# Kernel optimization log

Hardware: AMD Instinct MI355X
Metric: run time of the kernel (lower is better)

## Reference

```python
import jax, jax.numpy as jnp
import numpy as np

N = 131072   # total nodes in batch
D = 128      # hidden dim (in_dim = out_dim = 128)
DX = 64      # raw node feature dim (x and rw_feature each)
NG = 1024    # number of graphs (global_add_pool segments)
E = 4194304  # edges per hop adjacency (avg degree 32)
H = 4        # num_hops + 1 MLP branches per layer


def setup_inputs() -> dict:
    key = jax.random.key(0)
    ks = jax.random.split(key, 16)
    s = 0.05
    return {
        "x": jax.random.normal(ks[0], (N, DX), jnp.float32),
        "rw_feature": jax.random.normal(ks[1], (N, DX), jnp.float32),
        "hop1_features": jax.random.normal(ks[2], (N, D), jnp.float32),
        "hop2_features": jax.random.normal(ks[3], (N, D), jnp.float32),
        "hop3_features": jax.random.normal(ks[4], (N, D), jnp.float32),
        "hop1_edges": jax.random.randint(ks[5], (2, E), 0, N, dtype=jnp.int32),
        "hop2_edges": jax.random.randint(ks[6], (2, E), 0, N, dtype=jnp.int32),
        "hop3_edges": jax.random.randint(ks[7], (2, E), 0, N, dtype=jnp.int32),
        "batch": jnp.sort(jax.random.randint(ks[8], (N,), 0, NG, dtype=jnp.int32)),
        "l1_w1": jax.random.normal(ks[9], (H, D, D), jnp.float32) * s,
        "l1_b1": jnp.zeros((H, D), jnp.float32),
        "l1_w2": jax.random.normal(ks[10], (H, D, D), jnp.float32) * s,
        "l1_b2": jnp.zeros((H, D), jnp.float32),
        "l2_w1": jax.random.normal(ks[11], (H, D, D), jnp.float32) * s,
        "l2_b1": jnp.zeros((H, D), jnp.float32),
        "l2_w2": jax.random.normal(ks[12], (H, D, D), jnp.float32) * s,
        "l2_b2": jnp.zeros((H, D), jnp.float32),
        "lin_w": jax.random.normal(ks[13], (2 * D, D), jnp.float32) * s,
        "lin_b": jnp.zeros((D,), jnp.float32),
    }


def _mhc_layer(hops, w1, b1, w2, b2):
    # hops: [H, N, D]; per-hop MLP (Linear -> ReLU -> Dropout(eval) -> Linear), summed over hops
    z = jax.nn.relu(jnp.einsum('hni,hio->hno', hops, w1) + b1[:, None, :])
    y = jnp.einsum('hno,hop->hnp', z, w2) + b2[:, None, :]
    return jnp.sum(y, axis=0)  # [N, D]


def _spmm(edges, x):
    # torch.sparse.mm(A, x) with A[r, c] = 1.0 per edge; duplicate edges accumulate (COO sum)
    return jax.ops.segment_sum(x[edges[1]], edges[0], num_segments=N)


def reference(x, rw_feature, hop1_features, hop2_features, hop3_features,
              hop1_edges, hop2_edges, hop3_edges, batch,
              l1_w1, l1_b1, l1_w2, l1_b2, l2_w1, l2_b1, l2_w2, l2_b2,
              lin_w, lin_b):
    f = jnp.concatenate([x, rw_feature], axis=1)  # [N, D]
    h1 = jnp.stack([f, hop1_features, hop2_features, hop3_features], axis=0)  # [H, N, D]
    x1 = _mhc_layer(h1, l1_w1, l1_b1, l1_w2, l1_b2)
    h2 = jnp.stack([x1,
                    _spmm(hop1_edges, x1),
                    _spmm(hop2_edges, x1),
                    _spmm(hop3_edges, x1)], axis=0)
    x2 = _mhc_layer(h2, l2_w1, l2_b1, l2_w2, l2_b2)
    out = jnp.concatenate([x1, x2], axis=1) @ lin_w + lin_b  # concat=True path
    return jax.ops.segment_sum(out, batch, num_segments=NG)  # global_add_pool -> [NG, D]
```

## Files before the change

kernel.cpp:

```cpp
#include <hip/hip_runtime.h>

#define N_NODES 131072
#define DIM     128
#define NGRAPH  1024
#define NEDGE   4194304

#define NW      512
#define WBINS   256
#define NSL     256
#define SLICE_E (NEDGE / NSL)
#define CAP     12288

typedef float floatx4 __attribute__((ext_vector_type(4)));
typedef float f32x4  __attribute__((ext_vector_type(4)));
typedef __bf16 bf16x8 __attribute__((ext_vector_type(8)));
typedef __bf16 bf16x4 __attribute__((ext_vector_type(4)));

__device__ __forceinline__ int lds_off(int row, int kb) {
    return row * 256 + (kb ^ ((row & 7) << 4));
}

__global__ __launch_bounds__(256)
void zero_kernel(floatx4* __restrict__ p, long n4) {
    long i = (long)blockIdx.x * blockDim.x + threadIdx.x;
    long stride = (long)gridDim.x * blockDim.x;
    floatx4 z = {0.f, 0.f, 0.f, 0.f};
    for (; i < n4; i += stride) p[i] = z;
}

__global__ __launch_bounds__(256)
void tr_kernel(const float* __restrict__ src, __bf16* __restrict__ dst, int nmat) {
    int idx = blockIdx.x * blockDim.x + threadIdx.x;
    int total = nmat * 16384;
    if (idx >= total) return;
    int m = idx >> 14;
    int col = (idx >> 7) & 127;
    int k = idx & 127;
    dst[idx] = (__bf16)src[m * 16384 + k * 128 + col];
}

__global__ __launch_bounds__(256)
void wincount_kernel(const int* __restrict__ e1, const int* __restrict__ e2,
                     const int* __restrict__ e3, int* __restrict__ gcount) {
    const int gb = blockIdx.x;
    const int sl = gb % NSL;
    const int hop = gb / NSL;
    const int* rows = hop == 0 ? e1 : hop == 1 ? e2 : e3;

    __shared__ int cnt[NW];
    for (int i = threadIdx.x; i < NW; i += 256) cnt[i] = 0;
    __syncthreads();

    const int4* src = (const int4*)rows + (size_t)sl * (SLICE_E / 4);
    for (int j = threadIdx.x; j < SLICE_E / 4; j += 256) {
        int4 v = src[j];
        atomicAdd(&cnt[v.x >> 8], 1); atomicAdd(&cnt[v.y >> 8], 1);
        atomicAdd(&cnt[v.z >> 8], 1); atomicAdd(&cnt[v.w >> 8], 1);
    }
    __syncthreads();

    int* dst = gcount + ((size_t)hop * NSL + sl) * NW;
    for (int i = threadIdx.x; i < NW; i += 256) dst[i] = cnt[i];
}

__global__ __launch_bounds__(256)
void basescan_kernel(const int* __restrict__ gcount, int* __restrict__ baseo,
                     int* __restrict__ wbase) {
    const int hop = blockIdx.x;
    const int t = threadIdx.x;
    __shared__ int wt[NW];
    __shared__ int part[256];

    for (int k = 0; k < 2; ++k) {
        int w = t * 2 + k;
        int s = 0;
        for (int sl = 0; sl < NSL; ++sl)
            s += gcount[((size_t)hop * NSL + sl) * NW + w];
        wt[w] = s;
    }
    __syncthreads();
    part[t] = wt[2 * t] + wt[2 * t + 1];
    __syncthreads();
    for (int d = 1; d < 256; d <<= 1) {
        int v = (t >= d) ? part[t - d] : 0;
        __syncthreads();
        part[t] += v;
        __syncthreads();
    }
    int run = (t == 0) ? 0 : part[t - 1];
    for (int k = 0; k < 2; ++k) {
        int w = 2 * t + k;
        wbase[hop * (NW + 1) + w] = run;
        int r2 = run;
        for (int sl = 0; sl < NSL; ++sl) {
            baseo[((size_t)hop * NW + w) * NSL + sl] = r2;
            r2 += gcount[((size_t)hop * NSL + sl) * NW + w];
        }
        run += wt[w];
    }
    if (t == 255) wbase[hop * (NW + 1) + NW] = NEDGE;
}

__global__ __launch_bounds__(256)
void bucket_kernel(const int* __restrict__ e1, const int* __restrict__ e2,
                   const int* __restrict__ e3, const int* __restrict__ baseo,
                   int* __restrict__ buf) {
    const int gb = blockIdx.x;
    const int sl = gb % NSL;
    const int hop = gb / NSL;
    const int* rows = hop == 0 ? e1 : hop == 1 ? e2 : e3;
    const int* cs = rows + NEDGE;

    __shared__ int cur[NW];
    for (int i = threadIdx.x; i < NW; i += 256)
        cur[i] = baseo[((size_t)hop * NW + i) * NSL + sl];
    __syncthreads();

    int* b = buf + (size_t)hop * NEDGE;
    const int4* r4 = (const int4*)rows + (size_t)sl * (SLICE_E / 4);
    const int4* c4 = (const int4*)cs + (size_t)sl * (SLICE_E / 4);
    for (int j = threadIdx.x; j < SLICE_E / 4; j += 256) {
        int4 r = r4[j];
        int4 c = c4[j];
        int p;
        p = atomicAdd(&cur[r.x >> 8], 1); b[p] = ((r.x & 255) << 17) | c.x;
        p = atomicAdd(&cur[r.y >> 8], 1); b[p] = ((r.y & 255) << 17) | c.y;
        p = atomicAdd(&cur[r.z >> 8], 1); b[p] = ((r.z & 255) << 17) | c.z;
        p = atomicAdd(&cur[r.w >> 8], 1); b[p] = ((r.w & 255) << 17) | c.w;
    }
}

__global__ __launch_bounds__(256)
void winbuild_kernel(const int* __restrict__ buf, const int* __restrict__ wbase,
                     int* __restrict__ offs3, int* __restrict__ cols) {
    const int gb = blockIdx.x;
    const int w = gb % NW;
    const int hop = gb / NW;
    const int b0 = wbase[hop * (NW + 1) + w];
    const int b1 = wbase[hop * (NW + 1) + w + 1];
    const int tot = b1 - b0;
    const int* src = buf + (size_t)hop * NEDGE + b0;
    int* col = cols + (size_t)hop * NEDGE;
    int* offs = offs3 + (size_t)hop * (N_NODES + 1);
    const int t = threadIdx.x;

    __shared__ int hist[WBINS];
    __shared__ int scanb[WBINS];
    __shared__ int image[CAP];

    hist[t] = 0;
    __syncthreads();
    for (int i = t; i < tot; i += 256) atomicAdd(&hist[src[i] >> 17], 1);
    __syncthreads();

    int v = hist[t];
    scanb[t] = v;
    __syncthreads();
    for (int d = 1; d < 256; d <<= 1) {
        int u = (t >= d) ? scanb[t - d] : 0;
        __syncthreads();
        scanb[t] += u;
        __syncthreads();
    }
    const int excl = scanb[t] - v;

    offs[w * WBINS + t] = b0 + excl;
    if (w == NW - 1 && t == 0) offs[N_NODES] = NEDGE;
    __syncthreads();

    if (tot <= CAP) {
        hist[t] = excl;
        __syncthreads();
        for (int i = t; i < tot; i += 256) {
            int e = src[i];
            int p = atomicAdd(&hist[e >> 17], 1);
            image[p] = e & 0x1FFFF;
        }
        __syncthreads();
        for (int i = t; i < tot; i += 256) col[b0 + i] = image[i];
    } else {
        hist[t] = b0 + excl;
        __syncthreads();
        for (int i = t; i < tot; i += 256) {
            int e = src[i];
            int p = atomicAdd(&hist[e >> 17], 1);
            col[p] = e & 0x1FFFF;
        }
    }
}

__global__ __launch_bounds__(256)
void csr_spmm_kernel(const int* __restrict__ offs, const int* __restrict__ col,
                     const __bf16* __restrict__ xin, __bf16* __restrict__ outb) {
    const int lane = threadIdx.x & 63;
    const int row = blockIdx.x * (blockDim.x >> 6) + (threadIdx.x >> 6);
    if (row >= N_NODES) return;
    const int beg = offs[row];
    const int end = offs[row + 1];

    float a0 = 0.f, a1 = 0.f, b0 = 0.f, b1 = 0.f;
    float c0f = 0.f, c1f = 0.f, d0 = 0.f, d1 = 0.f;
    for (int b = beg; b < end; b += 64) {
        const int n = min(64, end - b);
        int cidx = (b + lane < end) ? col[b + lane] : 0;
        int i = 0;
        for (; i + 4 <= n; i += 4) {
            int e0 = __shfl(cidx, i);
            int e1 = __shfl(cidx, i + 1);
            int e2 = __shfl(cidx, i + 2);
            int e3 = __shfl(cidx, i + 3);
            unsigned v0 = *(const unsigned*)(xin + (size_t)e0 * 128 + lane * 2);
            unsigned v1 = *(const unsigned*)(xin + (size_t)e1 * 128 + lane * 2);
            unsigned v2 = *(const unsigned*)(xin + (size_t)e2 * 128 + lane * 2);
            unsigned v3 = *(const unsigned*)(xin + (size_t)e3 * 128 + lane * 2);
            a0 += __uint_as_float(v0 << 16); a1 += __uint_as_float(v0 & 0xffff0000u);
            b0 += __uint_as_float(v1 << 16); b1 += __uint_as_float(v1 & 0xffff0000u);
            c0f += __uint_as_float(v2 << 16); c1f += __uint_as_float(v2 & 0xffff0000u);
            d0 += __uint_as_float(v3 << 16); d1 += __uint_as_float(v3 & 0xffff0000u);
        }
        for (; i < n; ++i) {
            int e = __shfl(cidx, i);
            unsigned v = *(const unsigned*)(xin + (size_t)e * 128 + lane * 2);
            a0 += __uint_as_float(v << 16); a1 += __uint_as_float(v & 0xffff0000u);
        }
    }
    float o0 = a0 + b0 + c0f + d0;
    float o1 = a1 + b1 + c1f + d1;
    union { unsigned u; __bf16 h[2]; } pk;
    pk.h[0] = (__bf16)o0; pk.h[1] = (__bf16)o1;
    *(unsigned*)(outb + (size_t)row * 128 + lane * 2) = pk.u;
}

__device__ __forceinline__ void stage_bf16_tile(char* dst, const __bf16* src, int tid) {
#pragma unroll
    for (int it = 0; it < 8; ++it) {
        int c = tid + it * 256;
        int r = c >> 4, o = c & 15;
        uint4 v = *(const uint4*)(src + (size_t)r * 128 + o * 8);
        *(uint4*)(dst + lds_off(r, o * 16)) = v;
    }
}

__device__ __forceinline__ void stage_f32_tile(char* dst, const float* src, int tid) {
#pragma unroll
    for (int it = 0; it < 16; ++it) {
        int c = tid + it * 256;
        int r = c >> 5, o = c & 31;
        floatx4 v = *(const floatx4*)(src + (size_t)r * 128 + o * 4);
        bf16x4 h;
        h[0] = (__bf16)v[0]; h[1] = (__bf16)v[1];
        h[2] = (__bf16)v[2]; h[3] = (__bf16)v[3];
        *(bf16x4*)(dst + lds_off(r, o * 8)) = h;
    }
}

__device__ __forceinline__ void mfma_phase(const char* az, const char* wb,
                                           int r0, int lrow, int grp,
                                           f32x4 (&acc)[2][8]) {
    bf16x8 am[2][4];
#pragma unroll
    for (int mt = 0; mt < 2; ++mt)
#pragma unroll
        for (int kk = 0; kk < 4; ++kk)
            am[mt][kk] = *(const bf16x8*)(az + lds_off(r0 + mt * 16 + lrow,
                                                       kk * 64 + grp * 16));
#pragma unroll
    for (int kk = 0; kk < 4; ++kk)
#pragma unroll
        for (int n = 0; n < 8; ++n) {
            bf16x8 b = *(const bf16x8*)(wb + lds_off(n * 16 + lrow,
                                                     kk * 64 + grp * 16));
#pragma unroll
            for (int mt = 0; mt < 2; ++mt)
                acc[mt][n] = __builtin_amdgcn_mfma_f32_16x16x32_bf16(
                    am[mt][kk], b, acc[mt][n], 0, 0, 0);
        }
}

__global__ __launch_bounds__(256, 2)
void layer1_kernel(const float* __restrict__ x, const float* __restrict__ rw,
                   const float* __restrict__ f1, const float* __restrict__ f2,
                   const float* __restrict__ f3,
                   const __bf16* __restrict__ wt1, const float* __restrict__ b1,
                   const __bf16* __restrict__ wt2, const float* __restrict__ b2,
                   __bf16* __restrict__ x1out)
{
    __shared__ uint4 lds_u4[4096];
    char* AZ = (char*)lds_u4;
    char* WB = (char*)lds_u4 + 32768;
    const int tid = threadIdx.x;
    const int lane = tid & 63;
    const int w = tid >> 6;
    const int r0 = w * 32;
    const int lrow = lane & 15;
    const int grp = lane >> 4;
    const int row0 = blockIdx.x * 128;

    f32x4 Y[2][8];
#pragma unroll
    for (int mt = 0; mt < 2; ++mt)
#pragma unroll
        for (int n = 0; n < 8; ++n) Y[mt][n] = {0.f, 0.f, 0.f, 0.f};

    for (int h = 0; h < 4; ++h) {
        __syncthreads();
        if (h == 0) {
#pragma unroll
            for (int it = 0; it < 16; ++it) {
                int c = tid + it * 256;
                int r = c >> 5, o = c & 31;
                const float* src = (o < 16)
                    ? (x  + (size_t)(row0 + r) * 64 + o * 4)
                    : (rw + (size_t)(row0 + r) * 64 + (o - 16) * 4);
                floatx4 v = *(const floatx4*)src;
                bf16x4 hh;
                hh[0] = (__bf16)v[0]; hh[1] = (__bf16)v[1];
                hh[2] = (__bf16)v[2]; hh[3] = (__bf16)v[3];
                *(bf16x4*)(AZ + lds_off(r, o * 8)) = hh;
            }
        } else {
            const float* feat = (h == 1) ? f1 : (h == 2) ? f2 : f3;
            stage_f32_tile(AZ, feat + (size_t)row0 * 128, tid);
        }
        stage_bf16_tile(WB, wt1 + (size_t)h * 16384, tid);
        __syncthreads();

        f32x4 acc1[2][8];
#pragma unroll
        for (int mt = 0; mt < 2; ++mt)
#pragma unroll
            for (int n = 0; n < 8; ++n) acc1[mt][n] = {0.f, 0.f, 0.f, 0.f};
        mfma_phase(AZ, WB, r0, lrow, grp, acc1);

#pragma unroll
        for (int n = 0; n < 8; ++n) {
            float bias = b1[h * 128 + n * 16 + lrow];
#pragma unroll
            for (int mt = 0; mt < 2; ++mt)
#pragma unroll
                for (int rg = 0; rg < 4; ++rg) {
                    float v = fmaxf(acc1[mt][n][rg] + bias, 0.f);
                    int zr = r0 + mt * 16 + grp * 4 + rg;
                    *(__bf16*)(AZ + lds_off(zr, (n * 16 + lrow) * 2)) = (__bf16)v;
                }
        }
        __syncthreads();
        stage_bf16_tile(WB, wt2 + (size_t)h * 16384, tid);
        __syncthreads();
        mfma_phase(AZ, WB, r0, lrow, grp, Y);
    }

#pragma unroll
    for (int n = 0; n < 8; ++n) {
        int cc = n * 16 + lrow;
        float bs = b2[cc] + b2[128 + cc] + b2[256 + cc] + b2[384 + cc];
#pragma unroll
        for (int mt = 0; mt < 2; ++mt)
#pragma unroll
            for (int rg = 0; rg < 4; ++rg) {
                int gr = row0 + r0 + mt * 16 + grp * 4 + rg;
                x1out[(size_t)gr * 128 + cc] = (__bf16)(Y[mt][n][rg] + bs);
            }
    }
}

__global__ __launch_bounds__(256, 2)
void layer2_kernel(const __bf16* __restrict__ x1b, const __bf16* __restrict__ s1,
                   const __bf16* __restrict__ s2, const __bf16* __restrict__ s3,
                   const __bf16* __restrict__ wt1, const float* __restrict__ b1,
                   const __bf16* __restrict__ wt2, const float* __restrict__ b2,
                   const __bf16* __restrict__ wtl, const float* __restrict__ linb,
                   const int* __restrict__ batch, float* __restrict__ dout)
{
    __shared__ uint4 lds_u4[4096];
    char* AZ = (char*)lds_u4;
    char* WB = (char*)lds_u4 + 32768;
    const int tid = threadIdx.x;
    const int lane = tid & 63;
    const int w = tid >> 6;
    const int r0 = w * 32;
    const int lrow = lane & 15;
    const int grp = lane >> 4;
    const int row0 = blockIdx.x * 128;

    f32x4 Y[2][8];
#pragma unroll
    for (int mt = 0; mt < 2; ++mt)
#pragma unroll
        for (int n = 0; n < 8; ++n) Y[mt][n] = {0.f, 0.f, 0.f, 0.f};

    for (int h = 0; h < 4; ++h) {
        const __bf16* feat = (h == 0) ? x1b : (h == 1) ? s1 : (h == 2) ? s2 : s3;
        __syncthreads();
        stage_bf16_tile(AZ, feat + (size_t)row0 * 128, tid);
        stage_bf16_tile(WB, wt1 + (size_t)h * 16384, tid);
        __syncthreads();

        f32x4 acc1[2][8];
#pragma unroll
        for (int mt = 0; mt < 2; ++mt)
#pragma unroll
            for (int n = 0; n < 8; ++n) acc1[mt][n] = {0.f, 0.f, 0.f, 0.f};
        mfma_phase(AZ, WB, r0, lrow, grp, acc1);

#pragma unroll
        for (int n = 0; n < 8; ++n) {
            float bias = b1[h * 128 + n * 16 + lrow];
#pragma unroll
            for (int mt = 0; mt < 2; ++mt)
#pragma unroll
                for (int rg = 0; rg < 4; ++rg) {
                    float v = fmaxf(acc1[mt][n][rg] + bias, 0.f);
                    int zr = r0 + mt * 16 + grp * 4 + rg;
                    *(__bf16*)(AZ + lds_off(zr, (n * 16 + lrow) * 2)) = (__bf16)v;
                }
        }
        __syncthreads();
        stage_bf16_tile(WB, wt2 + (size_t)h * 16384, tid);
        __syncthreads();
        mfma_phase(AZ, WB, r0, lrow, grp, Y);
    }

#pragma unroll
    for (int n = 0; n < 8; ++n) {
        int cc = n * 16 + lrow;
        float bs = b2[cc] + b2[128 + cc] + b2[256 + cc] + b2[384 + cc];
#pragma unroll
        for (int mt = 0; mt < 2; ++mt)
#pragma unroll
            for (int rg = 0; rg < 4; ++rg) {
                float v = Y[mt][n][rg] + bs;
                int zr = r0 + mt * 16 + grp * 4 + rg;
                *(__bf16*)(AZ + lds_off(zr, (n * 16 + lrow) * 2)) = (__bf16)v;
            }
    }
    __syncthreads();
    stage_bf16_tile(WB, wtl + 16384, tid);
    __syncthreads();

    f32x4 o[2][8];
#pragma unroll
    for (int mt = 0; mt < 2; ++mt)
#pragma unroll
        for (int n = 0; n < 8; ++n) o[mt][n] = {0.f, 0.f, 0.f, 0.f};
    mfma_phase(AZ, WB, r0, lrow, grp, o);

    __syncthreads();
    stage_bf16_tile(AZ, x1b + (size_t)row0 * 128, tid);
    stage_bf16_tile(WB, wtl, tid);
    __syncthreads();
    mfma_phase(AZ, WB, r0, lrow, grp, o);

    __syncthreads();
    float* tile32 = (float*)lds_u4;
#pragma unroll
    for (int n = 0; n < 8; ++n) {
        int cc = n * 16 + lrow;
        float lb = linb[cc];
#pragma unroll
        for (int mt = 0; mt < 2; ++mt)
#pragma unroll
            for (int rg = 0; rg < 4; ++rg) {
                int rl = r0 + mt * 16 + grp * 4 + rg;
                tile32[rl * 128 + cc] = o[mt][n][rg] + lb;
            }
    }
    __syncthreads();

    if (tid < 128) {
        const int d = tid;
        float acc = 0.f;
        int cur = batch[row0];
        for (int r = 0; r < 128; ++r) {
            int b = batch[row0 + r];
            if (b != cur) {
                atomicAdd(dout + (size_t)cur * 128 + d, acc);
                acc = 0.f;
                cur = b;
            }
            acc += tile32[r * 128 + d];
        }
        atomicAdd(dout + (size_t)cur * 128 + d, acc);
    }
}

extern "C" void kernel_launch(void* const* d_in, const int* in_sizes, int n_in,
                              void* d_out, int out_size, void* d_ws, size_t ws_size,
                              hipStream_t stream) {
    (void)in_sizes; (void)n_in; (void)out_size; (void)ws_size;

    const float* x    = (const float*)d_in[0];
    const float* rw   = (const float*)d_in[1];
    const float* f1   = (const float*)d_in[2];
    const float* f2   = (const float*)d_in[3];
    const float* f3   = (const float*)d_in[4];
    const int*   e1   = (const int*)d_in[5];
    const int*   e2   = (const int*)d_in[6];
    const int*   e3   = (const int*)d_in[7];
    const int*   batch= (const int*)d_in[8];
    const float* l1w1 = (const float*)d_in[9];
    const float* l1b1 = (const float*)d_in[10];
    const float* l1w2 = (const float*)d_in[11];
    const float* l1b2 = (const float*)d_in[12];
    const float* l2w1 = (const float*)d_in[13];
    const float* l2b1 = (const float*)d_in[14];
    const float* l2w2 = (const float*)d_in[15];
    const float* l2b2 = (const float*)d_in[16];
    const float* linw = (const float*)d_in[17];
    const float* linb = (const float*)d_in[18];

    float* out = (float*)d_out;

    __bf16* x1b = (__bf16*)d_ws;
    __bf16* s1b = x1b + (size_t)N_NODES * 128;
    __bf16* s2b = s1b + (size_t)N_NODES * 128;
    __bf16* s3b = s2b + (size_t)N_NODES * 128;
    __bf16* wt  = s3b + (size_t)N_NODES * 128;
    __bf16* wt_l1w1 = wt;
    __bf16* wt_l1w2 = wt + 4 * 16384;
    __bf16* wt_l2w1 = wt + 8 * 16384;
    __bf16* wt_l2w2 = wt + 12 * 16384;
    __bf16* wt_lin  = wt + 16 * 16384;
    int* ibase  = (int*)(wt + 18 * 16384);
    int* offs3  = ibase;
    int* gcount = offs3 + (size_t)3 * (N_NODES + 1);
    int* baseo  = gcount + (size_t)3 * NSL * NW;
    int* wbase  = baseo + (size_t)3 * NW * NSL;
    int* buf    = wbase + (size_t)3 * (NW + 1);
    int* cols   = buf + (size_t)3 * NEDGE;

    tr_kernel<<<256, 256, 0, stream>>>(l1w1, wt_l1w1, 4);
    tr_kernel<<<256, 256, 0, stream>>>(l1w2, wt_l1w2, 4);
    tr_kernel<<<256, 256, 0, stream>>>(l2w1, wt_l2w1, 4);
    tr_kernel<<<256, 256, 0, stream>>>(l2w2, wt_l2w2, 4);
    tr_kernel<<<128, 256, 0, stream>>>(linw, wt_lin, 2);

    zero_kernel<<<64, 256, 0, stream>>>((floatx4*)out, (long)NGRAPH * 32);

    layer1_kernel<<<N_NODES / 128, 256, 0, stream>>>(
        x, rw, f1, f2, f3, wt_l1w1, l1b1, wt_l1w2, l1b2, x1b);

    wincount_kernel<<<3 * NSL, 256, 0, stream>>>(e1, e2, e3, gcount);
    basescan_kernel<<<3, 256, 0, stream>>>(gcount, baseo, wbase);
    bucket_kernel<<<3 * NSL, 256, 0, stream>>>(e1, e2, e3, baseo, buf);
    winbuild_kernel<<<3 * NW, 256, 0, stream>>>(buf, wbase, offs3, cols);

    __bf16* ss[3] = {s1b, s2b, s3b};
    for (int hop = 0; hop < 3; ++hop) {
        csr_spmm_kernel<<<N_NODES / 4, 256, 0, stream>>>(
            offs3 + (size_t)hop * (N_NODES + 1), cols + (size_t)hop * NEDGE,
            x1b, ss[hop]);
    }

    layer2_kernel<<<N_NODES / 128, 256, 0, stream>>>(
        x1b, s1b, s2b, s3b, wt_l2w1, l2b1, wt_l2w2, l2b2, wt_lin, linb, batch, out);
}
```

Before: 1.097 ms.

## Restructure MLP kernels to per-wave 16-row tiles with direct global operand loads

New measurement: 1.281 ms. 16.8% more time.

```diff
diff --git a/kernel.cpp b/kernel.cpp
--- a/kernel.cpp
+++ b/kernel.cpp
@@ -14,7 +14,6 @@
 typedef float floatx4 __attribute__((ext_vector_type(4)));
 typedef float f32x4  __attribute__((ext_vector_type(4)));
 typedef __bf16 bf16x8 __attribute__((ext_vector_type(8)));
-typedef __bf16 bf16x4 __attribute__((ext_vector_type(4)));
 
 __device__ __forceinline__ int lds_off(int row, int kb) {
     return row * 256 + (kb ^ ((row & 7) << 4));
@@ -231,53 +230,7 @@
     *(unsigned*)(outb + (size_t)row * 128 + lane * 2) = pk.u;
 }
 
-__device__ __forceinline__ void stage_bf16_tile(char* dst, const __bf16* src, int tid) {
-#pragma unroll
-    for (int it = 0; it < 8; ++it) {
-        int c = tid + it * 256;
-        int r = c >> 4, o = c & 15;
-        uint4 v = *(const uint4*)(src + (size_t)r * 128 + o * 8);
-        *(uint4*)(dst + lds_off(r, o * 16)) = v;
-    }
-}
-
-__device__ __forceinline__ void stage_f32_tile(char* dst, const float* src, int tid) {
-#pragma unroll
-    for (int it = 0; it < 16; ++it) {
-        int c = tid + it * 256;
-        int r = c >> 5, o = c & 31;
-        floatx4 v = *(const floatx4*)(src + (size_t)r * 128 + o * 4);
-        bf16x4 h;
-        h[0] = (__bf16)v[0]; h[1] = (__bf16)v[1];
-        h[2] = (__bf16)v[2]; h[3] = (__bf16)v[3];
-        *(bf16x4*)(dst + lds_off(r, o * 8)) = h;
-    }
-}
-
-__device__ __forceinline__ void mfma_phase(const char* az, const char* wb,
-                                           int r0, int lrow, int grp,
-                                           f32x4 (&acc)[2][8]) {
-    bf16x8 am[2][4];
-#pragma unroll
-    for (int mt = 0; mt < 2; ++mt)
-#pragma unroll
-        for (int kk = 0; kk < 4; ++kk)
-            am[mt][kk] = *(const bf16x8*)(az + lds_off(r0 + mt * 16 + lrow,
-                                                       kk * 64 + grp * 16));
-#pragma unroll
-    for (int kk = 0; kk < 4; ++kk)
-#pragma unroll
-        for (int n = 0; n < 8; ++n) {
-            bf16x8 b = *(const bf16x8*)(wb + lds_off(n * 16 + lrow,
-                                                     kk * 64 + grp * 16));
-#pragma unroll
-            for (int mt = 0; mt < 2; ++mt)
-                acc[mt][n] = __builtin_amdgcn_mfma_f32_16x16x32_bf16(
-                    am[mt][kk], b, acc[mt][n], 0, 0, 0);
-        }
-}
-
-__global__ __launch_bounds__(256, 2)
+__global__ __launch_bounds__(256, 3)
 void layer1_kernel(const float* __restrict__ x, const float* __restrict__ rw,
                    const float* __restrict__ f1, const float* __restrict__ f2,
                    const float* __restrict__ f3,
@@ -285,69 +238,85 @@
                    const __bf16* __restrict__ wt2, const float* __restrict__ b2,
                    __bf16* __restrict__ x1out)
 {
-    __shared__ uint4 lds_u4[4096];
-    char* AZ = (char*)lds_u4;
-    char* WB = (char*)lds_u4 + 32768;
+    __shared__ char zbuf[4][4096];
     const int tid = threadIdx.x;
     const int lane = tid & 63;
     const int w = tid >> 6;
-    const int r0 = w * 32;
     const int lrow = lane & 15;
     const int grp = lane >> 4;
-    const int row0 = blockIdx.x * 128;
-
-    f32x4 Y[2][8];
-#pragma unroll
-    for (int mt = 0; mt < 2; ++mt)
-#pragma unroll
-        for (int n = 0; n < 8; ++n) Y[mt][n] = {0.f, 0.f, 0.f, 0.f};
-
+    char* Z = zbuf[w];
+    const int row0 = blockIdx.x * 64;
+    const int grow = row0 + w * 16 + lrow;
+
+    f32x4 Y[8];
+#pragma unroll
+    for (int n = 0; n < 8; ++n) Y[n] = {0.f, 0.f, 0.f, 0.f};
+
+    const __bf16* w1base = wt1 + (size_t)lrow * 128 + grp * 8;
+    const __bf16* w2base = wt2 + (size_t)lrow * 128 + grp * 8;
+
+#pragma unroll
     for (int h = 0; h < 4; ++h) {
-        __syncthreads();
+        bf16x8 af[4];
         if (h == 0) {
 #pragma unroll
-            for (int it = 0; it < 16; ++it) {
-                int c = tid + it * 256;
-                int r = c >> 5, o = c & 31;
-                const float* src = (o < 16)
-                    ? (x  + (size_t)(row0 + r) * 64 + o * 4)
-                    : (rw + (size_t)(row0 + r) * 64 + (o - 16) * 4);
-                floatx4 v = *(const floatx4*)src;
-                bf16x4 hh;
-                hh[0] = (__bf16)v[0]; hh[1] = (__bf16)v[1];
-                hh[2] = (__bf16)v[2]; hh[3] = (__bf16)v[3];
-                *(bf16x4*)(AZ + lds_off(r, o * 8)) = hh;
+            for (int kk = 0; kk < 4; ++kk) {
+                const float* s = (kk < 2)
+                    ? (x  + (size_t)grow * 64 + kk * 32 + grp * 8)
+                    : (rw + (size_t)grow * 64 + (kk - 2) * 32 + grp * 8);
+                floatx4 v0 = *(const floatx4*)s;
+                floatx4 v1 = *(const floatx4*)(s + 4);
+#pragma unroll
+                for (int j = 0; j < 4; ++j) {
+                    af[kk][j] = (__bf16)v0[j]; af[kk][4 + j] = (__bf16)v1[j];
+                }
             }
         } else {
             const float* feat = (h == 1) ? f1 : (h == 2) ? f2 : f3;
-            stage_f32_tile(AZ, feat + (size_t)row0 * 128, tid);
-        }
-        stage_bf16_tile(WB, wt1 + (size_t)h * 16384, tid);
-        __syncthreads();
-
-        f32x4 acc1[2][8];
-#pragma unroll
-        for (int mt = 0; mt < 2; ++mt)
-#pragma unroll
-            for (int n = 0; n < 8; ++n) acc1[mt][n] = {0.f, 0.f, 0.f, 0.f};
-        mfma_phase(AZ, WB, r0, lrow, grp, acc1);
+            const float* s0 = feat + (size_t)grow * 128 + grp * 8;
+#pragma unroll
+            for (int kk = 0; kk < 4; ++kk) {
+                floatx4 v0 = *(const floatx4*)(s0 + kk * 32);
+                floatx4 v1 = *(const floatx4*)(s0 + kk * 32 + 4);
+#pragma unroll
+                for (int j = 0; j < 4; ++j) {
+                    af[kk][j] = (__bf16)v0[j]; af[kk][4 + j] = (__bf16)v1[j];
+                }
+            }
+        }
+
+        f32x4 acc[8];
+#pragma unroll
+        for (int n = 0; n < 8; ++n) acc[n] = {0.f, 0.f, 0.f, 0.f};
+        const __bf16* w1h = w1base + (size_t)h * 16384;
+#pragma unroll
+        for (int kk = 0; kk < 4; ++kk)
+#pragma unroll
+            for (int n = 0; n < 8; ++n) {
+                bf16x8 bf = *(const bf16x8*)(w1h + n * 2048 + kk * 32);
+                acc[n] = __builtin_amdgcn_mfma_f32_16x16x32_bf16(af[kk], bf, acc[n], 0, 0, 0);
+            }
 
 #pragma unroll
         for (int n = 0; n < 8; ++n) {
             float bias = b1[h * 128 + n * 16 + lrow];
 #pragma unroll
-            for (int mt = 0; mt < 2; ++mt)
-#pragma unroll
-                for (int rg = 0; rg < 4; ++rg) {
-                    float v = fmaxf(acc1[mt][n][rg] + bias, 0.f);
-                    int zr = r0 + mt * 16 + grp * 4 + rg;
-                    *(__bf16*)(AZ + lds_off(zr, (n * 16 + lrow) * 2)) = (__bf16)v;
-                }
-        }
-        __syncthreads();
-        stage_bf16_tile(WB, wt2 + (size_t)h * 16384, tid);
-        __syncthreads();
-        mfma_phase(AZ, WB, r0, lrow, grp, Y);
+            for (int rg = 0; rg < 4; ++rg) {
+                float v = fmaxf(acc[n][rg] + bias, 0.f);
+                *(__bf16*)(Z + lds_off(grp * 4 + rg, (n * 16 + lrow) * 2)) = (__bf16)v;
+            }
+        }
+
+        const __bf16* w2h = w2base + (size_t)h * 16384;
+#pragma unroll
+        for (int kk = 0; kk < 4; ++kk) {
+            bf16x8 a2 = *(const bf16x8*)(Z + lds_off(lrow, kk * 64 + grp * 16));
+#pragma unroll
+            for (int n = 0; n < 8; ++n) {
+                bf16x8 bf = *(const bf16x8*)(w2h + n * 2048 + kk * 32);
+                Y[n] = __builtin_amdgcn_mfma_f32_16x16x32_bf16(a2, bf, Y[n], 0, 0, 0);
+            }
+        }
     }
 
 #pragma unroll
@@ -355,16 +324,19 @@
         int cc = n * 16 + lrow;
         float bs = b2[cc] + b2[128 + cc] + b2[256 + cc] + b2[384 + cc];
 #pragma unroll
-        for (int mt = 0; mt < 2; ++mt)
-#pragma unroll
-            for (int rg = 0; rg < 4; ++rg) {
-                int gr = row0 + r0 + mt * 16 + grp * 4 + rg;
-                x1out[(size_t)gr * 128 + cc] = (__bf16)(Y[mt][n][rg] + bs);
-            }
-    }
-}
-
-__global__ __launch_bounds__(256, 2)
+        for (int rg = 0; rg < 4; ++rg)
+            *(__bf16*)(Z + lds_off(grp * 4 + rg, cc * 2)) = (__bf16)(Y[n][rg] + bs);
+    }
+#pragma unroll
+    for (int it = 0; it < 4; ++it) {
+        int f = it * 64 + lane;
+        int r = f >> 4, o = f & 15;
+        uint4 v = *(const uint4*)(Z + lds_off(r, o * 16));
+        *(uint4*)(x1out + (size_t)(row0 + w * 16 + r) * 128 + o * 8) = v;
+    }
+}
+
+__global__ __launch_bounds__(256, 3)
 void layer2_kernel(const __bf16* __restrict__ x1b, const __bf16* __restrict__ s1,
                    const __bf16* __restrict__ s2, const __bf16* __restrict__ s3,
                    const __bf16* __restrict__ wt1, const float* __restrict__ b1,
@@ -372,53 +344,64 @@
                    const __bf16* __restrict__ wtl, const float* __restrict__ linb,
                    const int* __restrict__ batch, float* __restrict__ dout)
 {
-    __shared__ uint4 lds_u4[4096];
-    char* AZ = (char*)lds_u4;
-    char* WB = (char*)lds_u4 + 32768;
+    __shared__ char zbuf[4][4096];
     const int tid = threadIdx.x;
     const int lane = tid & 63;
     const int w = tid >> 6;
-    const int r0 = w * 32;
     const int lrow = lane & 15;
     const int grp = lane >> 4;
-    const int row0 = blockIdx.x * 128;
-
-    f32x4 Y[2][8];
-#pragma unroll
-    for (int mt = 0; mt < 2; ++mt)
-#pragma unroll
-        for (int n = 0; n < 8; ++n) Y[mt][n] = {0.f, 0.f, 0.f, 0.f};
-
+    char* Z = zbuf[w];
+    const int row0 = blockIdx.x * 64;
+    const int grow = row0 + w * 16 + lrow;
+
+    f32x4 Y[8];
+#pragma unroll
+    for (int n = 0; n < 8; ++n) Y[n] = {0.f, 0.f, 0.f, 0.f};
+
+    const __bf16* w1base = wt1 + (size_t)lrow * 128 + grp * 8;
+    const __bf16* w2base = wt2 + (size_t)lrow * 128 + grp * 8;
+
+#pragma unroll
     for (int h = 0; h < 4; ++h) {
         const __bf16* feat = (h == 0) ? x1b : (h == 1) ? s1 : (h == 2) ? s2 : s3;
-        __syncthreads();
-        stage_bf16_tile(AZ, feat + (size_t)row0 * 128, tid);
-        stage_bf16_tile(WB, wt1 + (size_t)h * 16384, tid);
-        __syncthreads();
-
-        f32x4 acc1[2][8];
-#pragma unroll
-        for (int mt = 0; mt < 2; ++mt)
-#pragma unroll
-            for (int n = 0; n < 8; ++n) acc1[mt][n] = {0.f, 0.f, 0.f, 0.f};
-        mfma_phase(AZ, WB, r0, lrow, grp, acc1);
+        const __bf16* s0 = feat + (size_t)grow * 128 + grp * 8;
+        bf16x8 af[4];
+#pragma unroll
+        for (int kk = 0; kk < 4; ++kk)
+            af[kk] = *(const bf16x8*)(s0 + kk * 32);
+
+        f32x4 acc[8];
+#pragma unroll
+        for (int n = 0; n < 8; ++n) acc[n] = {0.f, 0.f, 0.f, 0.f};
+        const __bf16* w1h = w1base + (size_t)h * 16384;
+#pragma unroll
+        for (int kk = 0; kk < 4; ++kk)
+#pragma unroll
+            for (int n = 0; n < 8; ++n) {
+                bf16x8 bf = *(const bf16x8*)(w1h + n * 2048 + kk * 32);
+                acc[n] = __builtin_amdgcn_mfma_f32_16x16x32_bf16(af[kk], bf, acc[n], 0, 0, 0);
+            }
 
 #pragma unroll
         for (int n = 0; n < 8; ++n) {
             float bias = b1[h * 128 + n * 16 + lrow];
 #pragma unroll
-            for (int mt = 0; mt < 2; ++mt)
-#pragma unroll
-                for (int rg = 0; rg < 4; ++rg) {
-                    float v = fmaxf(acc1[mt][n][rg] + bias, 0.f);
-                    int zr = r0 + mt * 16 + grp * 4 + rg;
-                    *(__bf16*)(AZ + lds_off(zr, (n * 16 + lrow) * 2)) = (__bf16)v;
-                }
-        }
-        __syncthreads();
-        stage_bf16_tile(WB, wt2 + (size_t)h * 16384, tid);
-        __syncthreads();
-        mfma_phase(AZ, WB, r0, lrow, grp, Y);
+            for (int rg = 0; rg < 4; ++rg) {
+                float v = fmaxf(acc[n][rg] + bias, 0.f);
+                *(__bf16*)(Z + lds_off(grp * 4 + rg, (n * 16 + lrow) * 2)) = (__bf16)v;
+            }
+        }
+
+        const __bf16* w2h = w2base + (size_t)h * 16384;
+#pragma unroll
+        for (int kk = 0; kk < 4; ++kk) {
+            bf16x8 a2 = *(const bf16x8*)(Z + lds_off(lrow, kk * 64 + grp * 16));
+#pragma unroll
+            for (int n = 0; n < 8; ++n) {
+                bf16x8 bf = *(const bf16x8*)(w2h + n * 2048 + kk * 32);
+                Y[n] = __builtin_amdgcn_mfma_f32_16x16x32_bf16(a2, bf, Y[n], 0, 0, 0);
+            }
+        }
     }
 
 #pragma unroll
@@ -426,59 +409,59 @@
         int cc = n * 16 + lrow;
         float bs = b2[cc] + b2[128 + cc] + b2[256 + cc] + b2[384 + cc];
 #pragma unroll
-        for (int mt = 0; mt < 2; ++mt)
-#pragma unroll
-            for (int rg = 0; rg < 4; ++rg) {
-                float v = Y[mt][n][rg] + bs;
-                int zr = r0 + mt * 16 + grp * 4 + rg;
-                *(__bf16*)(AZ + lds_off(zr, (n * 16 + lrow) * 2)) = (__bf16)v;
-            }
-    }
-    __syncthreads();
-    stage_bf16_tile(WB, wtl + 16384, tid);
-    __syncthreads();
-
-    f32x4 o[2][8];
-#pragma unroll
-    for (int mt = 0; mt < 2; ++mt)
-#pragma unroll
-        for (int n = 0; n < 8; ++n) o[mt][n] = {0.f, 0.f, 0.f, 0.f};
-    mfma_phase(AZ, WB, r0, lrow, grp, o);
-
-    __syncthreads();
-    stage_bf16_tile(AZ, x1b + (size_t)row0 * 128, tid);
-    stage_bf16_tile(WB, wtl, tid);
-    __syncthreads();
-    mfma_phase(AZ, WB, r0, lrow, grp, o);
-
-    __syncthreads();
-    float* tile32 = (float*)lds_u4;
+        for (int rg = 0; rg < 4; ++rg)
+            *(__bf16*)(Z + lds_off(grp * 4 + rg, cc * 2)) = (__bf16)(Y[n][rg] + bs);
+    }
+
+    f32x4 o[8];
+#pragma unroll
+    for (int n = 0; n < 8; ++n) o[n] = {0.f, 0.f, 0.f, 0.f};
+
+    const __bf16* wl1 = wtl + 16384 + (size_t)lrow * 128 + grp * 8;
+#pragma unroll
+    for (int kk = 0; kk < 4; ++kk) {
+        bf16x8 a2 = *(const bf16x8*)(Z + lds_off(lrow, kk * 64 + grp * 16));
+#pragma unroll
+        for (int n = 0; n < 8; ++n) {
+            bf16x8 bf = *(const bf16x8*)(wl1 + n * 2048 + kk * 32);
+            o[n] = __builtin_amdgcn_mfma_f32_16x16x32_bf16(a2, bf, o[n], 0, 0, 0);
+        }
+    }
+    const __bf16* wl0 = wtl + (size_t)lrow * 128 + grp * 8;
+    const __bf16* xs = x1b + (size_t)grow * 128 + grp * 8;
+#pragma unroll
+    for (int kk = 0; kk < 4; ++kk) {
+        bf16x8 a1 = *(const bf16x8*)(xs + kk * 32);
+#pragma unroll
+        for (int n = 0; n < 8; ++n) {
+            bf16x8 bf = *(const bf16x8*)(wl0 + n * 2048 + kk * 32);
+            o[n] = __builtin_amdgcn_mfma_f32_16x16x32_bf16(a1, bf, o[n], 0, 0, 0);
+        }
+    }
+
 #pragma unroll
     for (int n = 0; n < 8; ++n) {
         int cc = n * 16 + lrow;
         float lb = linb[cc];
 #pragma unroll
-        for (int mt = 0; mt < 2; ++mt)
-#pragma unroll
-            for (int rg = 0; rg < 4; ++rg) {
-                int rl = r0 + mt * 16 + grp * 4 + rg;
-                tile32[rl * 128 + cc] = o[mt][n][rg] + lb;
-            }
+        for (int rg = 0; rg < 4; ++rg)
+            *(__bf16*)(Z + lds_off(grp * 4 + rg, cc * 2)) = (__bf16)(o[n][rg] + lb);
     }
     __syncthreads();
 
     if (tid < 128) {
         const int d = tid;
+        const char* zf = &zbuf[0][0];
         float acc = 0.f;
         int cur = batch[row0];
-        for (int r = 0; r < 128; ++r) {
+        for (int r = 0; r < 64; ++r) {
             int b = batch[row0 + r];
             if (b != cur) {
                 atomicAdd(dout + (size_t)cur * 128 + d, acc);
                 acc = 0.f;
                 cur = b;
             }
-            acc += tile32[r * 128 + d];
+            acc += (float)*(const __bf16*)(zf + r * 256 + ((d * 2) ^ ((r & 7) << 4)));
         }
         atomicAdd(dout + (size_t)cur * 128 + d, acc);
     }
@@ -537,7 +520,7 @@
 
     zero_kernel<<<64, 256, 0, stream>>>((floatx4*)out, (long)NGRAPH * 32);
 
-    layer1_kernel<<<N_NODES / 128, 256, 0, stream>>>(
+    layer1_kernel<<<N_NODES / 64, 256, 0, stream>>>(
         x, rw, f1, f2, f3, wt_l1w1, l1b1, wt_l1w2, l1b2, x1b);
 
     wincount_kernel<<<3 * NSL, 256, 0, stream>>>(e1, e2, e3, gcount);
@@ -552,6 +535,6 @@
             x1b, ss[hop]);
     }
 
-    layer2_kernel<<<N_NODES / 128, 256, 0, stream>>>(
+    layer2_kernel<<<N_NODES / 64, 256, 0, stream>>>(
         x1b, s1b, s2b, s3b, wt_l2w1, l2b1, wt_l2w2, l2b2, wt_lin, linb, batch, out);
 }
```

## Read MLP weights directly from global memory instead of staging them in LDS

Applied to the files above, without the earlier changes.

After: 1.219 ms. 11.2% more time.

```diff
diff --git a/kernel.cpp b/kernel.cpp
--- a/kernel.cpp
+++ b/kernel.cpp
@@ -254,9 +254,9 @@
     }
 }
 
-__device__ __forceinline__ void mfma_phase(const char* az, const char* wb,
-                                           int r0, int lrow, int grp,
-                                           f32x4 (&acc)[2][8]) {
+__device__ __forceinline__ void mfma_phase_g(const char* az, const __bf16* wb,
+                                             int r0, int lrow, int grp,
+                                             f32x4 (&acc)[2][8]) {
     bf16x8 am[2][4];
 #pragma unroll
     for (int mt = 0; mt < 2; ++mt)
@@ -268,8 +268,7 @@
     for (int kk = 0; kk < 4; ++kk)
 #pragma unroll
         for (int n = 0; n < 8; ++n) {
-            bf16x8 b = *(const bf16x8*)(wb + lds_off(n * 16 + lrow,
-                                                     kk * 64 + grp * 16));
+            bf16x8 b = *(const bf16x8*)(wb + n * 2048 + kk * 32);
 #pragma unroll
             for (int mt = 0; mt < 2; ++mt)
                 acc[mt][n] = __builtin_amdgcn_mfma_f32_16x16x32_bf16(
@@ -285,9 +284,7 @@
                    const __bf16* __restrict__ wt2, const float* __restrict__ b2,
                    __bf16* __restrict__ x1out)
 {
-    __shared__ uint4 lds_u4[4096];
-    char* AZ = (char*)lds_u4;
-    char* WB = (char*)lds_u4 + 32768;
+    __shared__ char AZ[32768];
     const int tid = threadIdx.x;
     const int lane = tid & 63;
     const int w = tid >> 6;
@@ -301,6 +298,9 @@
     for (int mt = 0; mt < 2; ++mt)
 #pragma unroll
         for (int n = 0; n < 8; ++n) Y[mt][n] = {0.f, 0.f, 0.f, 0.f};
+
+    const __bf16* w1base = wt1 + (size_t)lrow * 128 + grp * 8;
+    const __bf16* w2base = wt2 + (size_t)lrow * 128 + grp * 8;
 
     for (int h = 0; h < 4; ++h) {
         __syncthreads();
@@ -322,15 +322,14 @@
             const float* feat = (h == 1) ? f1 : (h == 2) ? f2 : f3;
             stage_f32_tile(AZ, feat + (size_t)row0 * 128, tid);
         }
-        stage_bf16_tile(WB, wt1 + (size_t)h * 16384, tid);
-        __syncthreads();
-
-        f32x4 acc1[2][8];
+        __syncthreads();
+
+        f32x4 acc[2][8];
 #pragma unroll
         for (int mt = 0; mt < 2; ++mt)
 #pragma unroll
-            for (int n = 0; n < 8; ++n) acc1[mt][n] = {0.f, 0.f, 0.f, 0.f};
-        mfma_phase(AZ, WB, r0, lrow, grp, acc1);
+            for (int n = 0; n < 8; ++n) acc[mt][n] = {0.f, 0.f, 0.f, 0.f};
+        mfma_phase_g(AZ, w1base + (size_t)h * 16384, r0, lrow, grp, acc);
 
 #pragma unroll
         for (int n = 0; n < 8; ++n) {
@@ -339,15 +338,13 @@
             for (int mt = 0; mt < 2; ++mt)
 #pragma unroll
                 for (int rg = 0; rg < 4; ++rg) {
-                    float v = fmaxf(acc1[mt][n][rg] + bias, 0.f);
+                    float v = fmaxf(acc[mt][n][rg] + bias, 0.f);
                     int zr = r0 + mt * 16 + grp * 4 + rg;
                     *(__bf16*)(AZ + lds_off(zr, (n * 16 + lrow) * 2)) = (__bf16)v;
                 }
         }
-        __syncthreads();
-        stage_bf16_tile(WB, wt2 + (size_t)h * 16384, tid);
-        __syncthreads();
-        mfma_phase(AZ, WB, r0, lrow, grp, Y);
+
+        mfma_phase_g(AZ, w2base + (size_t)h * 16384, r0, lrow, grp, Y);
     }
 
 #pragma unroll
@@ -358,9 +355,16 @@
         for (int mt = 0; mt < 2; ++mt)
 #pragma unroll
             for (int rg = 0; rg < 4; ++rg) {
-                int gr = row0 + r0 + mt * 16 + grp * 4 + rg;
-                x1out[(size_t)gr * 128 + cc] = (__bf16)(Y[mt][n][rg] + bs);
+                int zr = r0 + mt * 16 + grp * 4 + rg;
+                *(__bf16*)(AZ + lds_off(zr, cc * 2)) = (__bf16)(Y[mt][n][rg] + bs);
             }
+    }
+#pragma unroll
+    for (int it = 0; it < 8; ++it) {
+        int f = it * 64 + lane;
+        int r = f >> 4, o = f & 15;
+        uint4 v = *(const uint4*)(AZ + lds_off(r0 + r, o * 16));
+        *(uint4*)(x1out + (size_t)(row0 + r0 + r) * 128 + o * 8) = v;
     }
 }
 
@@ -372,9 +376,7 @@
                    const __bf16* __restrict__ wtl, const float* __restrict__ linb,
                    const int* __restrict__ batch, float* __restrict__ dout)
 {
-    __shared__ uint4 lds_u4[4096];
-    char* AZ = (char*)lds_u4;
-    char* WB = (char*)lds_u4 + 32768;
+    __shared__ char AZ[32768];
     const int tid = threadIdx.x;
     const int lane = tid & 63;
     const int w = tid >> 6;
@@ -389,19 +391,21 @@
 #pragma unroll
         for (int n = 0; n < 8; ++n) Y[mt][n] = {0.f, 0.f, 0.f, 0.f};
 
+    const __bf16* w1base = wt1 + (size_t)lrow * 128 + grp * 8;
+    const __bf16* w2base = wt2 + (size_t)lrow * 128 + grp * 8;
+
     for (int h = 0; h < 4; ++h) {
         const __bf16* feat = (h == 0) ? x1b : (h == 1) ? s1 : (h == 2) ? s2 : s3;
         __syncthreads();
         stage_bf16_tile(AZ, feat + (size_t)row0 * 128, tid);
-        stage_bf16_tile(WB, wt1 + (size_t)h * 16384, tid);
-        __syncthreads();
-
-        f32x4 acc1[2][8];
+        __syncthreads();
+
+        f32x4 acc[2][8];
 #pragma unroll
         for (int mt = 0; mt < 2; ++mt)
 #pragma unroll
-            for (int n = 0; n < 8; ++n) acc1[mt][n] = {0.f, 0.f, 0.f, 0.f};
-        mfma_phase(AZ, WB, r0, lrow, grp, acc1);
+            for (int n = 0; n < 8; ++n) acc[mt][n] = {0.f, 0.f, 0.f, 0.f};
+        mfma_phase_g(AZ, w1base + (size_t)h * 16384, r0, lrow, grp, acc);
 
 #pragma unroll
         for (int n = 0; n < 8; ++n) {
@@ -410,15 +414,12 @@
             for (int mt = 0; mt < 2; ++mt)
 #pragma unroll
                 for (int rg = 0; rg < 4; ++rg) {
-                    float v = fmaxf(acc1[mt][n][rg] + bias, 0.f);
+                    float v = fmaxf(acc[mt][n][rg] + bias, 0.f);
                     int zr = r0 + mt * 16 + grp * 4 + rg;
                     *(__bf16*)(AZ + lds_off(zr, (n * 16 + lrow) * 2)) = (__bf16)v;
                 }
         }
-        __syncthreads();
-        stage_bf16_tile(WB, wt2 + (size_t)h * 16384, tid);
-        __syncthreads();
-        mfma_phase(AZ, WB, r0, lrow, grp, Y);
+        mfma_phase_g(AZ, w2base + (size_t)h * 16384, r0, lrow, grp, Y);
     }
 
 #pragma unroll
@@ -429,30 +430,23 @@
         for (int mt = 0; mt < 2; ++mt)
 #pragma unroll
             for (int rg = 0; rg < 4; ++rg) {
-                float v = Y[mt][n][rg] + bs;
                 int zr = r0 + mt * 16 + grp * 4 + rg;
-                *(__bf16*)(AZ + lds_off(zr, (n * 16 + lrow) * 2)) = (__bf16)v;
+                *(__bf16*)(AZ + lds_off(zr, cc * 2)) = (__bf16)(Y[mt][n][rg] + bs);
             }
     }
-    __syncthreads();
-    stage_bf16_tile(WB, wtl + 16384, tid);
-    __syncthreads();
 
     f32x4 o[2][8];
 #pragma unroll
     for (int mt = 0; mt < 2; ++mt)
 #pragma unroll
         for (int n = 0; n < 8; ++n) o[mt][n] = {0.f, 0.f, 0.f, 0.f};
-    mfma_phase(AZ, WB, r0, lrow, grp, o);
+    mfma_phase_g(AZ, wtl + 16384 + (size_t)lrow * 128 + grp * 8, r0, lrow, grp, o);
 
     __syncthreads();
     stage_bf16_tile(AZ, x1b + (size_t)row0 * 128, tid);
-    stage_bf16_tile(WB, wtl, tid);
-    __syncthreads();
-    mfma_phase(AZ, WB, r0, lrow, grp, o);
-
-    __syncthreads();
-    float* tile32 = (float*)lds_u4;
+    __syncthreads();
+    mfma_phase_g(AZ, wtl + (size_t)lrow * 128 + grp * 8, r0, lrow, grp, o);
+
 #pragma unroll
     for (int n = 0; n < 8; ++n) {
         int cc = n * 16 + lrow;
@@ -461,8 +455,8 @@
         for (int mt = 0; mt < 2; ++mt)
 #pragma unroll
             for (int rg = 0; rg < 4; ++rg) {
-                int rl = r0 + mt * 16 + grp * 4 + rg;
-                tile32[rl * 128 + cc] = o[mt][n][rg] + lb;
+                int zr = r0 + mt * 16 + grp * 4 + rg;
+                *(__bf16*)(AZ + lds_off(zr, cc * 2)) = (__bf16)(o[mt][n][rg] + lb);
             }
     }
     __syncthreads();
@@ -478,7 +472,7 @@
                 acc = 0.f;
                 cur = b;
             }
-            acc += tile32[r * 128 + d];
+            acc += (float)*(const __bf16*)(AZ + r * 256 + ((d * 2) ^ ((r & 7) << 4)));
         }
         atomicAdd(dout + (size_t)cur * 128 + d, acc);
     }
```
